# Kernel optimization log

Measured on AMD Instinct MI355X. Metric: run time of the kernel, lower is better.

The kernel has to match this reference:

```python
import jax, jax.numpy as jnp
import numpy as np

B, N, COOR, F, FILT = 8, 128, 3, 128, 128


def setup_inputs() -> dict:
    key = jax.random.key(0)
    k1, k2, k3, k4 = jax.random.split(key, 4)
    return {
        "vector_features": jax.random.normal(k1, (B, N, COOR, F), dtype=jnp.float32),
        "distances": jax.random.normal(k2, (B, N, N, COOR), dtype=jnp.float32),
        "w_vs": jax.random.normal(k3, (2 * F, FILT), dtype=jnp.float32) * 0.05,
        "b_vs": jax.random.normal(k4, (FILT,), dtype=jnp.float32) * 0.05,
    }


def reference(vector_features, distances, w_vs, b_vs):
    # Original tiles x to [B,N,N,coor,F], transposes for the pair partner,
    # concats along features, and matmuls with w_vs [2F, filt].
    # concat([x_i, x_j]) @ w_vs == x_i @ w_vs[:F] + x_j @ w_vs[F:], so we
    # avoid materializing the [B,N,N,coor,2F] tile.
    f = vector_features.shape[-1]
    a = jnp.einsum('bncf,fk->bnck', vector_features, w_vs[:f])   # i-part
    c = jnp.einsum('bncf,fk->bnck', vector_features, w_vs[f:])   # j-part
    # pairwise: [B, N(i), N(j), coor, filt]
    pair = a[:, :, None, :, :] + c[:, None, :, :, :] + b_vs
    # distance-weighted reduction over coor axis -> [B, N, N, filt]
    scalar = jnp.sum(pair * distances[..., None], axis=-2)
    # activation=None -> linear
    return scalar
```

## Files before the change

kernel.cpp:

```cpp
#include <hip/hip_runtime.h>

#define BB   8
#define NN   128
#define FF   128
#define KK   128

typedef float f32x4 __attribute__((ext_vector_type(4)));

__global__ __launch_bounds__(256) void k_pre(const float* __restrict__ vf,
                                             const float* __restrict__ w,
                                             const float* __restrict__ bias,
                                             float* __restrict__ ac) {
    const int bn0 = blockIdx.x * 2;
    const int tid = threadIdx.x;
    const int col  = tid & 127;
    const int half = tid >> 7;
    const float* wcol = w + half * (FF * KK) + col;
    const float* vr = vf + (size_t)bn0 * 384;

    float a00 = 0.f, a01 = 0.f, a02 = 0.f;
    float a10 = 0.f, a11 = 0.f, a12 = 0.f;
#pragma unroll 8
    for (int f = 0; f < FF; ++f) {
        const float wv = wcol[f * KK];
        a00 = fmaf(wv, vr[f],       a00);
        a01 = fmaf(wv, vr[128 + f], a01);
        a02 = fmaf(wv, vr[256 + f], a02);
        a10 = fmaf(wv, vr[384 + f], a10);
        a11 = fmaf(wv, vr[512 + f], a11);
        a12 = fmaf(wv, vr[640 + f], a12);
    }
    const float hb = 0.5f * bias[col];
    float* dst = ac + (size_t)bn0 * 768 + half * 128 + col;
    dst[0]    = a00 + hb;  dst[256]  = a01 + hb;  dst[512]  = a02 + hb;
    dst[768]  = a10 + hb;  dst[1024] = a11 + hb;  dst[1280] = a12 + hb;
}

__global__ __launch_bounds__(256) void k_main(const float* __restrict__ dist,
                                              const float* __restrict__ ac,
                                              float* __restrict__ out) {
    const int bx  = blockIdx.x;
    const int b   = bx >> 8;
    const int rem = bx & 255;
    const int it  = rem >> 3;
    const int jt  = rem & 7;
    const int i0  = it * 4, j0 = jt * 16;
    const int tid = threadIdx.x;

    __shared__ float dl[192];
    if (tid < 192) {
        const int ti = tid / 48, r = tid % 48;
        dl[tid] = dist[((size_t)(b * NN + i0 + ti) * NN + j0) * 3 + r];
    }
    __syncthreads();

    const int k4 = tid & 31;
    const int rg = tid >> 5;
    const int ti = rg >> 1;
    const int jp = rg & 1;
    const int i  = i0 + ti;

    const float4* arow = (const float4*)(ac + (size_t)(b * NN + i) * 768) + k4;
    const float4 a0 = arow[0], a1 = arow[64], a2 = arow[128];
    float* obase = out + (size_t)(b * NN + i) * NN * KK;
    const float* dlt = dl + ti * 48;

#pragma unroll
    for (int p = 0; p < 8; ++p) {
        const int jj = 2 * p + jp;
        const int j  = j0 + jj;
        const float d0 = dlt[jj * 3], d1 = dlt[jj * 3 + 1], d2 = dlt[jj * 3 + 2];

        const float4* crow = (const float4*)(ac + (size_t)(b * NN + j) * 768)
                             + 32 + k4;
        const float4 c0 = crow[0], c1 = crow[64], c2 = crow[128];

        f32x4 r;
        r.x = fmaf(d0, a0.x + c0.x, fmaf(d1, a1.x + c1.x, d2 * (a2.x + c2.x)));
        r.y = fmaf(d0, a0.y + c0.y, fmaf(d1, a1.y + c1.y, d2 * (a2.y + c2.y)));
        r.z = fmaf(d0, a0.z + c0.z, fmaf(d1, a1.z + c1.z, d2 * (a2.z + c2.z)));
        r.w = fmaf(d0, a0.w + c0.w, fmaf(d1, a1.w + c1.w, d2 * (a2.w + c2.w)));

        __builtin_nontemporal_store(r, (f32x4*)(obase + (size_t)j * KK + k4 * 4));
    }
}

__global__ __launch_bounds__(256) void k_fused_slow(const float* __restrict__ vf,
                                                    const float* __restrict__ dist,
                                                    const float* __restrict__ w,
                                                    const float* __restrict__ bias,
                                                    float* __restrict__ out) {
    const int bi  = blockIdx.x;
    const int b   = bi >> 7;
    const int tid = threadIdx.x;
    __shared__ float arow[384];
    __shared__ float crow[384];

    for (int idx = tid; idx < 384; idx += 256) {
        const int c = idx >> 7, k = idx & 127;
        const float* v = vf + (size_t)bi * 384 + c * 128;
        float s = 0.f;
        for (int f = 0; f < 128; ++f) s = fmaf(v[f], w[f * 128 + k], s);
        arow[idx] = s;
    }
    __syncthreads();

    for (int j = 0; j < NN; ++j) {
        for (int idx = tid; idx < 384; idx += 256) {
            const int c = idx >> 7, k = idx & 127;
            const float* v = vf + (size_t)(b * NN + j) * 384 + c * 128;
            float s = 0.f;
            for (int f = 0; f < 128; ++f) s = fmaf(v[f], w[(128 + f) * 128 + k], s);
            crow[idx] = s;
        }
        __syncthreads();
        if (tid < 128) {
            const float* dj = dist + ((size_t)bi * NN + j) * 3;
            const float d0 = dj[0], d1 = dj[1], d2 = dj[2];
            const float sd = d0 + d1 + d2;
            const float r = fmaf(d0, arow[tid] + crow[tid],
                            fmaf(d1, arow[128 + tid] + crow[128 + tid],
                            fmaf(d2, arow[256 + tid] + crow[256 + tid], sd * bias[tid])));
            out[((size_t)bi * NN + j) * 128 + tid] = r;
        }
        __syncthreads();
    }
}

extern "C" void kernel_launch(void* const* d_in, const int* in_sizes, int n_in,
                              void* d_out, int out_size, void* d_ws, size_t ws_size,
                              hipStream_t stream) {
    const float* vf   = (const float*)d_in[0];
    const float* dist = (const float*)d_in[1];
    const float* w    = (const float*)d_in[2];
    const float* bias = (const float*)d_in[3];
    float* out = (float*)d_out;

    const size_t need = (size_t)BB * NN * 3 * 256 * sizeof(float);
    if (ws_size >= need) {
        float* ac = (float*)d_ws;
        k_pre<<<512, 256, 0, stream>>>(vf, w, bias, ac);
        k_main<<<2048, 256, 0, stream>>>(dist, ac, out);
    } else {
        k_fused_slow<<<BB * NN, 256, 0, stream>>>(vf, dist, w, bias, out);
    }
}
```

Measured before the change: 26.54 us.

## Restructure precompute kernel with LDS-staged inputs, vectorized weights, split-F reduction

The projection precompute kernel now stages the two input rows in shared memory and has each thread compute four output columns with float4 weight loads. The feature dimension is split in half across thread groups, and the two partial sums are combined through a shared-memory reduction. Previously each thread did scalar strided weight loads for six outputs. This aims to cut global load instructions and latency in k_pre, at the cost of an extra barrier and LDS traffic; k_main is unchanged.

```diff
diff --git a/kernel.cpp b/kernel.cpp
--- a/kernel.cpp
+++ b/kernel.cpp
@@ -13,27 +13,50 @@
                                              float* __restrict__ ac) {
     const int bn0 = blockIdx.x * 2;
     const int tid = threadIdx.x;
-    const int col  = tid & 127;
-    const int half = tid >> 7;
-    const float* wcol = w + half * (FF * KK) + col;
-    const float* vr = vf + (size_t)bn0 * 384;
+    __shared__ __align__(16) float vfr[768];
+    __shared__ f32x4 red[128][3];
 
-    float a00 = 0.f, a01 = 0.f, a02 = 0.f;
-    float a10 = 0.f, a11 = 0.f, a12 = 0.f;
-#pragma unroll 8
-    for (int f = 0; f < FF; ++f) {
-        const float wv = wcol[f * KK];
-        a00 = fmaf(wv, vr[f],       a00);
-        a01 = fmaf(wv, vr[128 + f], a01);
-        a02 = fmaf(wv, vr[256 + f], a02);
-        a10 = fmaf(wv, vr[384 + f], a10);
-        a11 = fmaf(wv, vr[512 + f], a11);
-        a12 = fmaf(wv, vr[640 + f], a12);
+    if (tid < 192) {
+        ((f32x4*)vfr)[tid] = ((const f32x4*)(vf + (size_t)bn0 * 384))[tid];
     }
-    const float hb = 0.5f * bias[col];
-    float* dst = ac + (size_t)bn0 * 768 + half * 128 + col;
-    dst[0]    = a00 + hb;  dst[256]  = a01 + hb;  dst[512]  = a02 + hb;
-    dst[768]  = a10 + hb;  dst[1024] = a11 + hb;  dst[1280] = a12 + hb;
+    __syncthreads();
+
+    const int kq = tid & 63;
+    const int fh = (tid >> 6) & 1;
+    const int r  = tid >> 7;
+    const int wrow0 = (kq < 32 ? 0 : 128) + fh * 64;
+    const int wcol  = (kq & 31) * 4;
+    const float* wp = w + (size_t)wrow0 * KK + wcol;
+    const float* vp = vfr + r * 384 + fh * 64;
+
+    f32x4 acc0 = {0.f,0.f,0.f,0.f}, acc1 = acc0, acc2 = acc0;
+#pragma unroll 2
+    for (int g = 0; g < 16; ++g) {
+        const int f = g * 4;
+        const f32x4 w0 = *(const f32x4*)(wp + (size_t)(f + 0) * KK);
+        const f32x4 w1 = *(const f32x4*)(wp + (size_t)(f + 1) * KK);
+        const f32x4 w2 = *(const f32x4*)(wp + (size_t)(f + 2) * KK);
+        const f32x4 w3 = *(const f32x4*)(wp + (size_t)(f + 3) * KK);
+        const f32x4 v0 = *(const f32x4*)(vp + f);
+        const f32x4 v1 = *(const f32x4*)(vp + 128 + f);
+        const f32x4 v2 = *(const f32x4*)(vp + 256 + f);
+        acc0 += w0 * v0.x + w1 * v0.y + w2 * v0.z + w3 * v0.w;
+        acc1 += w0 * v1.x + w1 * v1.y + w2 * v1.z + w3 * v1.w;
+        acc2 += w0 * v2.x + w1 * v2.y + w2 * v2.z + w3 * v2.w;
+    }
+
+    const int slot = r * 64 + kq;
+    if (fh) {
+        red[slot][0] = acc0; red[slot][1] = acc1; red[slot][2] = acc2;
+    }
+    __syncthreads();
+    if (!fh) {
+        const f32x4 hb = 0.5f * *(const f32x4*)(bias + (kq & 31) * 4);
+        f32x4* dst = (f32x4*)(ac + (size_t)(bn0 + r) * 768) + kq;
+        dst[0]   = acc0 + red[slot][0] + hb;
+        dst[64]  = acc1 + red[slot][1] + hb;
+        dst[128] = acc2 + red[slot][2] + hb;
+    }
 }
 
 __global__ __launch_bounds__(256) void k_main(const float* __restrict__ dist,
```

Measured after the change: 28.43 us. 7.1% more time.

## Compute per-node projections with bf16 MFMA instead of scalar FMA loops

Applied to the files above, without the earlier changes.

Replaces the scalar-FMA projection kernel with a bf16 matrix-core kernel. It converts vector features and weight tiles to bf16 in LDS and uses 16x16x32 MFMA to produce the i- and j-part projections. This targets the compute cost of the small pre-GEMM, at the price of bf16 rounding of inputs, which may exceed tolerance. The main pairwise kernel, which writes the large output and likely dominates runtime, is unchanged.

```diff
diff --git a/kernel.cpp b/kernel.cpp
--- a/kernel.cpp
+++ b/kernel.cpp
@@ -5,35 +5,82 @@
 #define FF   128
 #define KK   128
 
-typedef float f32x4 __attribute__((ext_vector_type(4)));
+typedef float  f32x4  __attribute__((ext_vector_type(4)));
+typedef short  bf16x8 __attribute__((ext_vector_type(8)));
+typedef short  short4v __attribute__((ext_vector_type(4)));
 
-__global__ __launch_bounds__(256) void k_pre(const float* __restrict__ vf,
-                                             const float* __restrict__ w,
-                                             const float* __restrict__ bias,
-                                             float* __restrict__ ac) {
-    const int bn0 = blockIdx.x * 2;
+__device__ __forceinline__ short f2bf(float x) {
+    union { float f; unsigned u; } v; v.f = x;
+    unsigned u = v.u + (0x7fffu + ((v.u >> 16) & 1u));
+    return (short)(u >> 16);
+}
+
+#define LROW 136
+
+__global__ __launch_bounds__(256) void k_pre_mfma(const float* __restrict__ vf,
+                                                  const float* __restrict__ w,
+                                                  const float* __restrict__ bias,
+                                                  float* __restrict__ ac) {
+    const int bx  = blockIdx.x;
+    const int mt  = bx >> 2;
+    const int ntq = bx & 3;
     const int tid = threadIdx.x;
-    const int col  = tid & 127;
-    const int half = tid >> 7;
-    const float* wcol = w + half * (FF * KK) + col;
-    const float* vr = vf + (size_t)bn0 * 384;
 
-    float a00 = 0.f, a01 = 0.f, a02 = 0.f;
-    float a10 = 0.f, a11 = 0.f, a12 = 0.f;
-#pragma unroll 8
-    for (int f = 0; f < FF; ++f) {
-        const float wv = wcol[f * KK];
-        a00 = fmaf(wv, vr[f],       a00);
-        a01 = fmaf(wv, vr[128 + f], a01);
-        a02 = fmaf(wv, vr[256 + f], a02);
-        a10 = fmaf(wv, vr[384 + f], a10);
-        a11 = fmaf(wv, vr[512 + f], a11);
-        a12 = fmaf(wv, vr[640 + f], a12);
+    __shared__ short a_lds[16 * LROW];
+    __shared__ short b_lds[64 * LROW];
+
+    {
+        const f32x4* vfp = (const f32x4*)vf + (size_t)mt * 512;
+        const int m  = tid >> 4;
+        const int k0 = (tid & 15) * 8;
+#pragma unroll
+        for (int q = 0; q < 2; ++q) {
+            const f32x4 v = vfp[tid * 2 + q];
+            short4v s;
+            s.x = f2bf(v.x); s.y = f2bf(v.y); s.z = f2bf(v.z); s.w = f2bf(v.w);
+            *(short4v*)(&a_lds[m * LROW + k0 + q * 4]) = s;
+        }
     }
-    const float hb = 0.5f * bias[col];
-    float* dst = ac + (size_t)bn0 * 768 + half * 128 + col;
-    dst[0]    = a00 + hb;  dst[256]  = a01 + hb;  dst[512]  = a02 + hb;
-    dst[768]  = a10 + hb;  dst[1024] = a11 + hb;  dst[1280] = a12 + hb;
+    {
+        const int whalf = ntq >> 1;
+        const int wcol0 = (ntq & 1) * 64;
+        const int kloc  = tid >> 4;
+        const int cq    = tid & 15;
+#pragma unroll
+        for (int kb = 0; kb < 8; ++kb) {
+            const int k = kb * 16 + kloc;
+            const f32x4 v = *(const f32x4*)(w + (size_t)(whalf * 128 + k) * KK
+                                              + wcol0 + cq * 4);
+            b_lds[(cq * 4 + 0) * LROW + k] = f2bf(v.x);
+            b_lds[(cq * 4 + 1) * LROW + k] = f2bf(v.y);
+            b_lds[(cq * 4 + 2) * LROW + k] = f2bf(v.z);
+            b_lds[(cq * 4 + 3) * LROW + k] = f2bf(v.w);
+        }
+    }
+    __syncthreads();
+
+    const int wid  = tid >> 6;
+    const int lane = tid & 63;
+    const int lg   = lane >> 4;
+    const int ln   = lane & 15;
+    const int nt   = ntq * 4 + wid;
+
+    f32x4 acc = {0.f, 0.f, 0.f, 0.f};
+#pragma unroll
+    for (int s = 0; s < 4; ++s) {
+        const int k0 = s * 32 + lg * 8;
+        const bf16x8 af = *(const bf16x8*)(&a_lds[ln * LROW + k0]);
+        const bf16x8 bf = *(const bf16x8*)(&b_lds[(wid * 16 + ln) * LROW + k0]);
+        acc = __builtin_amdgcn_mfma_f32_16x16x32_bf16(af, bf, acc, 0, 0, 0);
+    }
+
+    const int ncol = nt * 16 + ln;
+    const float hb = 0.5f * bias[ncol & 127];
+#pragma unroll
+    for (int r = 0; r < 4; ++r) {
+        const int mrow = mt * 16 + lg * 4 + r;
+        ac[(size_t)mrow * 256 + ncol] = acc[r] + hb;
+    }
 }
 
 __global__ __launch_bounds__(256) void k_main(const float* __restrict__ dist,
@@ -139,7 +186,7 @@
     const size_t need = (size_t)BB * NN * 3 * 256 * sizeof(float);
     if (ws_size >= need) {
         float* ac = (float*)d_ws;
-        k_pre<<<512, 256, 0, stream>>>(vf, w, bias, ac);
+        k_pre_mfma<<<768, 256, 0, stream>>>(vf, w, bias, ac);
         k_main<<<2048, 256, 0, stream>>>(dist, ac, out);
     } else {
         k_fused_slow<<<BB * NN, 256, 0, stream>>>(vf, dist, w, bias, out);
```

New measurement: 25.21 us. 1.05x faster.
